# Kernel tuning notes

Hardware: AMD Instinct MI355X
Metric: run time of the kernel (lower is better)

## Reference

```python
import jax, jax.numpy as jnp
import numpy as np

RES = 0.1
TABLE = 2 ** 20
MOD_T = 201
HEADS = 8
M = 500_000
D = 120
PRIMES_NP = np.array([73856093, 19349669, 83492791], dtype=np.int64)
BMIN = np.array([-2.6, -8.1, 0.0], dtype=np.float32)
BMAX = np.array([4.6, 4.7, 3.1], dtype=np.float32)
CORNERS = [(0, 0, 0), (1, 0, 0), (0, 1, 0), (0, 0, 1), (1, 1, 0), (1, 0, 1), (0, 1, 1), (1, 1, 1)]


def _build_hash_table():
    # Mirror torch.arange / meshgrid voxel grid construction.
    xs = np.arange(BMIN[0], BMAX[0], RES, dtype=np.float32)
    ys = np.arange(BMIN[1], BMAX[1], RES, dtype=np.float32)
    zs = np.arange(BMIN[2], BMAX[2], RES, dtype=np.float32)
    gx, gy, gz = np.meshgrid(xs, ys, zs, indexing='ij')
    vox = np.stack([gx, gy, gz], axis=-1).reshape(-1, 3)
    grid = np.floor(vox / RES).astype(np.int64)
    h = np.remainder((grid * PRIMES_NP).sum(-1), TABLE)
    buf = np.full(TABLE, -1, dtype=np.int64)
    uh, first_idx = np.unique(h, return_index=True)
    buf[uh] = first_idx
    return buf, vox.shape[0]


def setup_inputs() -> dict:
    key = jax.random.key(0)
    ks = jax.random.split(key, 12)
    buf_np, total_voxels = _build_hash_table()
    u = jax.random.uniform(ks[0], (M, 3), dtype=jnp.float32)
    query_pts = jnp.asarray(BMIN) + u * jnp.asarray(BMAX - BMIN)
    query_times = jax.random.randint(ks[1], (M,), 0, 1000, dtype=jnp.int64)
    dynamic_features = jax.random.normal(ks[2], (total_voxels, D), dtype=jnp.float32) * 0.01
    time_embeddings = jax.random.normal(ks[3], (MOD_T, D), dtype=jnp.float32) * 0.01
    s = 1.0 / np.sqrt(D)
    Wq = jax.random.normal(ks[4], (D, D), dtype=jnp.float32) * s
    Wk = jax.random.normal(ks[5], (D, D), dtype=jnp.float32) * s
    Wv = jax.random.normal(ks[6], (D, D), dtype=jnp.float32) * s
    Wo = jax.random.normal(ks[7], (D, D), dtype=jnp.float32) * s
    bq = jnp.zeros((D,), jnp.float32)
    bk = jnp.zeros((D,), jnp.float32)
    bv = jnp.zeros((D,), jnp.float32)
    bo = jnp.zeros((D,), jnp.float32)
    return {
        'query_pts': query_pts, 'query_times': query_times,
        'dynamic_features': dynamic_features, 'time_embeddings': time_embeddings,
        'buffer_voxel_index': jnp.asarray(buf_np),
        'Wq': Wq, 'bq': bq, 'Wk': Wk, 'bk': bk, 'Wv': Wv, 'bv': bv, 'Wo': Wo, 'bo': bo,
    }


def _attn_fuse(feat, time_emb, Wq, bq, Wk, bk, Wv, bv, Wo, bo):
    # 2-token self-attention fusion: tokens = [voxel feature, time embedding]
    m, d = feat.shape
    dh = d // HEADS
    x = jnp.stack([feat, time_emb], axis=1)  # (M, 2, D)
    q = (x @ Wq + bq).reshape(m, 2, HEADS, dh)
    k = (x @ Wk + bk).reshape(m, 2, HEADS, dh)
    v = (x @ Wv + bv).reshape(m, 2, HEADS, dh)
    scores = jnp.einsum('mqhd,mkhd->mhqk', q, k) / jnp.sqrt(jnp.float32(dh))
    a = jax.nn.softmax(scores, axis=-1)
    o = jnp.einsum('mhqk,mkhd->mqhd', a, v).reshape(m, 2, d)
    o = o @ Wo + bo
    return o.mean(axis=1)  # (M, D)


def reference(query_pts, query_times, dynamic_features, time_embeddings,
              buffer_voxel_index, Wq, bq, Wk, bk, Wv, bv, Wo, bo):
    primes = jnp.asarray(PRIMES_NP)
    m = query_pts.shape[0]
    d = dynamic_features.shape[1]
    t_mod = jnp.remainder(query_times, MOD_T)

    gf = query_pts / RES
    gfl = jnp.floor(gf)
    frac = gf - gfl                      # (M, 3)
    base = gfl.astype(jnp.int64)         # (M, 3)

    accum = jnp.zeros((m, d), dtype=query_pts.dtype)
    for ox, oy, oz in CORNERS:           # fixed structural 8-corner loop
        cc = base + jnp.asarray([ox, oy, oz], dtype=jnp.int64)
        h = jnp.remainder((cc * primes).sum(-1), TABLE)
        vidx = buffer_voxel_index[h]
        valid = vidx >= 0
        wx = frac[:, 0] if ox else 1.0 - frac[:, 0]
        wy = frac[:, 1] if oy else 1.0 - frac[:, 1]
        wz = frac[:, 2] if oz else 1.0 - frac[:, 2]
        w = wx * wy * wz                 # (M,)
        f = dynamic_features[jnp.where(valid, vidx, 0)]
        accum = accum + jnp.where(valid[:, None], f * w[:, None], 0.0)

    time_emb = time_embeddings[t_mod]
    return _attn_fuse(accum, time_emb, Wq, bq, Wk, bk, Wv, bv, Wo, bo)
```

## Files before the change

kernel.cpp:

```cpp
#include <hip/hip_runtime.h>
#include <math.h>

#define M_D   120
#define MOD_T 201
#define TABLE_MASK 0xFFFFFu
#define INV_S 0.25819888974716115f

#define WS_TV  1608
#define WS_TQK 27336
#define WS_DYN16_BYTE (1ull << 20)

typedef float    f32x4 __attribute__((ext_vector_type(4)));
typedef uint32_t u32x4 __attribute__((ext_vector_type(4)));
typedef __fp16   f16x2v __attribute__((ext_vector_type(2)));
typedef __fp16   f16x8 __attribute__((ext_vector_type(8)));

union PK2 { f16x2v h; uint32_t u; };
union BFrag { f16x8 v; f16x2v h2[4]; uint32_t u[4]; };

__global__ void precomp_time(const float* __restrict__ temb,
                             const float* __restrict__ Wq, const float* __restrict__ bq,
                             const float* __restrict__ Wk, const float* __restrict__ bk,
                             const float* __restrict__ Wv, const float* __restrict__ bv,
                             float* __restrict__ ws) {
  const int t = blockIdx.x, np = threadIdx.x;
  const int h = np >> 4, m = np & 15;
  const bool valid = (m < 15);
  const int col = h * 15 + m;
  __shared__ float lq[128], lk[128];
  float q = 0.f, k = 0.f, v = 0.f;
  if (valid) {
    q = bq[col]; k = bk[col]; v = bv[col];
    const float* te = temb + t * M_D;
    for (int i = 0; i < M_D; ++i) {
      float x = te[i];
      q = fmaf(x, Wq[i * M_D + col], q);
      k = fmaf(x, Wk[i * M_D + col], k);
      v = fmaf(x, Wv[i * M_D + col], v);
    }
  }
  lq[np] = q; lk[np] = k;
  ws[WS_TV + t * 128 + np] = v;
  PK2 pk; pk.h[0] = (__fp16)(q * INV_S); pk.h[1] = (__fp16)k;
  ((uint32_t*)ws)[WS_TQK + t * 128 + np] = pk.u;
  __syncthreads();
  if (np < 8) {
    float s = 0.f;
    #pragma unroll
    for (int mm = 0; mm < 15; ++mm) s += lq[np * 16 + mm] * lk[np * 16 + mm];
    ws[t * 8 + np] = s * INV_S;
  }
}

__global__ void cvt_dyn(const float* __restrict__ dyn, __fp16* __restrict__ d16, int rows) {
  const int i = blockIdx.x * 256 + threadIdx.x;
  const int row = i >> 4, sub = i & 15;
  if (row < rows) {
    BFrag o;
    if (sub == 15) { o.u[0] = 0; o.u[1] = 0; o.u[2] = 0; o.u[3] = 0; }
    else {
      const float* src = dyn + (long)row * M_D + sub * 8;
      const f32x4 a = __builtin_nontemporal_load((const f32x4*)src);
      const f32x4 b = __builtin_nontemporal_load((const f32x4*)(src + 4));
      o.h2[0] = __builtin_amdgcn_cvt_pkrtz(a[0], a[1]);
      o.h2[1] = __builtin_amdgcn_cvt_pkrtz(a[2], a[3]);
      o.h2[2] = __builtin_amdgcn_cvt_pkrtz(b[0], b[1]);
      o.h2[3] = __builtin_amdgcn_cvt_pkrtz(b[2], b[3]);
    }
    *(f16x8*)(d16 + (long)row * 128 + sub * 8) = o.v;
  }
}

__launch_bounds__(256, 2)
__global__ void gather_feat(const float* __restrict__ qpts, const __fp16* __restrict__ dyn16,
                            const int* __restrict__ hbuf, __fp16* __restrict__ feat, int M) {
  const int l = threadIdx.x & 63, wv = threadIdx.x >> 6;
  const int g = l >> 4, pl = l & 15;
  const int T = (M + 15) >> 4;
  for (int tile = blockIdx.x * 4 + wv; tile < T; tile += gridDim.x * 4) {
    const int pid = (tile << 4) + pl;
    const int p = (pid < M) ? pid : (M - 1);
    const float px = qpts[3 * p], py = qpts[3 * p + 1], pz = qpts[3 * p + 2];
    const float gx = px / 0.1f, gy = py / 0.1f, gz = pz / 0.1f;
    const float fx = floorf(gx), fy = floorf(gy), fz = floorf(gz);
    const float rx = gx - fx, ry = gy - fy, rz = gz - fz;
    const int bx = (int)fx, by = (int)fy, bz = (int)fz;

    int voff[8]; float wcv[8];
    #pragma unroll
    for (int c = 0; c < 8; ++c) {
      const int ox = c & 1, oy = (c >> 1) & 1, oz = c >> 2;
      const uint32_t hh = (uint32_t)(bx + ox) * 73856093u +
                          (uint32_t)(by + oy) * 19349669u +
                          (uint32_t)(bz + oz) * 83492791u;
      const int vc = hbuf[hh & TABLE_MASK];
      const float wc = (ox ? rx : 1.f - rx) * (oy ? ry : 1.f - ry) * (oz ? rz : 1.f - rz);
      wcv[c] = (vc >= 0) ? wc : 0.f;
      voff[c] = ((vc >= 0) ? vc : 0) * 128 + g * 8;
    }

    __fp16* frow = feat + (long)pid * 128 + g * 8;
    f16x8 va[8], vb[8];
    #pragma unroll
    for (int c = 0; c < 8; ++c) va[c] = *(const f16x8*)(dyn16 + voff[c]);
    #pragma unroll
    for (int c = 0; c < 8; ++c) vb[c] = *(const f16x8*)(dyn16 + voff[c] + 32);

    auto PROC = [&](int kk, f16x8* vk) {
      f32x4 accA = {0, 0, 0, 0}, accB = {0, 0, 0, 0};
      #pragma unroll
      for (int c = 0; c < 8; ++c) {
        const float wc = wcv[c];
        const f16x8 v8 = vk[c];
        accA[0] = fmaf((float)v8[0], wc, accA[0]);
        accA[1] = fmaf((float)v8[1], wc, accA[1]);
        accA[2] = fmaf((float)v8[2], wc, accA[2]);
        accA[3] = fmaf((float)v8[3], wc, accA[3]);
        accB[0] = fmaf((float)v8[4], wc, accB[0]);
        accB[1] = fmaf((float)v8[5], wc, accB[1]);
        accB[2] = fmaf((float)v8[6], wc, accB[2]);
        accB[3] = fmaf((float)v8[7], wc, accB[3]);
      }
      if (kk == 3 && g == 3) accA[0] = 1.0f;
      BFrag o;
      o.h2[0] = __builtin_amdgcn_cvt_pkrtz(accA[0], accA[1]);
      o.h2[1] = __builtin_amdgcn_cvt_pkrtz(accA[2], accA[3]);
      o.h2[2] = __builtin_amdgcn_cvt_pkrtz(accB[0], accB[1]);
      o.h2[3] = __builtin_amdgcn_cvt_pkrtz(accB[2], accB[3]);
      if (pid < M) *(f16x8*)(frow + kk * 32) = o.v;
    };

    PROC(0, va);
    #pragma unroll
    for (int c = 0; c < 8; ++c) va[c] = *(const f16x8*)(dyn16 + voff[c] + 64);
    PROC(1, vb);
    #pragma unroll
    for (int c = 0; c < 8; ++c) vb[c] = *(const f16x8*)(dyn16 + voff[c] + 96);
    PROC(2, va);
    PROC(3, vb);
  }
}

__launch_bounds__(512, 2)
__global__ void mfma_main(const int* __restrict__ qtimes, const __fp16* __restrict__ feat,
                          const float* __restrict__ Wq, const float* __restrict__ bq,
                          const float* __restrict__ Wk, const float* __restrict__ bk,
                          const float* __restrict__ Wv, const float* __restrict__ bv,
                          const float* __restrict__ Wo, const float* __restrict__ bo,
                          const float* __restrict__ ws, float* __restrict__ out, int M) {
  __shared__ __align__(16) uint32_t wlds[4 * 8192];

  const int tid = threadIdx.x;
  for (int idx = tid; idx < 32768; idx += 512) {
    const int mat = idx >> 13, r = idx & 8191;
    const int nt = r >> 10, kk = (r >> 8) & 3, l = (r >> 2) & 63, d = r & 3;
    const int mm = l & 15;
    const int i0 = kk * 32 + ((l >> 4) << 3) + 2 * d;
    float v0 = 0.f, v1 = 0.f;
    if (mat < 3) {
      const float* W = (mat == 0) ? Wq : (mat == 1) ? Wk : Wv;
      const float* b = (mat == 0) ? bq : (mat == 1) ? bk : bv;
      if (mm < 15) {
        const int col = nt * 15 + mm;
        const int ia = i0, ib = i0 + 1;
        v0 = (ia < 120) ? W[ia * M_D + col] : (ia == 120 ? b[col] : 0.f);
        v1 = (ib < 120) ? W[ib * M_D + col] : (ib == 120 ? b[col] : 0.f);
        if (mat == 0) { v0 *= INV_S; v1 *= INV_S; }
      }
    } else {
      const int n = nt * 16 + mm;
      if (n < M_D) {
        #pragma unroll
        for (int e = 0; e < 2; ++e) {
          const int ip = i0 + e;
          const int hi = ip >> 4, mi = ip & 15;
          float vv = 0.f;
          if (mi < 15) vv = Wo[(hi * 15 + mi) * M_D + n];
          else if (ip == 15) vv = bo[n];
          if (e == 0) v0 = vv; else v1 = vv;
        }
      }
    }
    PK2 pk; pk.h[0] = (__fp16)v0; pk.h[1] = (__fp16)v1;
    wlds[idx] = pk.u;
  }
  __syncthreads();

  const uint32_t* wq = wlds;
  const uint32_t* wk = wlds + 8192;
  const uint32_t* wvm = wlds + 2 * 8192;
  const uint32_t* wo = wlds + 3 * 8192;

  const int l = tid & 63, wv = tid >> 6;
  const int g = l >> 4, pl = l & 15, c0 = g << 2;
  const float* S11 = ws;
  const float* TVt = ws + WS_TV;
  const uint32_t* TQK = (const uint32_t*)ws + WS_TQK;

  const int T = (M + 15) >> 4;
  for (int tile = blockIdx.x * 8 + wv; tile < T; tile += gridDim.x * 8) {
    const int pid = (tile << 4) + pl;
    const bool valid = (pid < M);
    const int p = valid ? pid : (M - 1);
    const int tm = qtimes[p] % MOD_T;

    BFrag bf[4];
    const __fp16* frow = feat + (long)p * 128 + g * 8;
    #pragma unroll
    for (int kk = 0; kk < 4; ++kk) bf[kk].v = *(const f16x8*)(frow + kk * 32);

    f32x4 tvv[8]; u32x4 tqk[8]; float s11v[8];
    #pragma unroll
    for (int nt = 0; nt < 8; ++nt) {
      tvv[nt] = *(const f32x4*)(TVt + tm * 128 + nt * 16 + c0);
      tqk[nt] = *(const u32x4*)(TQK + tm * 128 + nt * 16 + c0);
      s11v[nt] = S11[tm * 8 + nt];
    }

    f32x4 aq[8], ak[8], av[8];
    #pragma unroll
    for (int nt = 0; nt < 8; ++nt) {
      f32x4 zq = {0,0,0,0}, zk = {0,0,0,0}, zv = {0,0,0,0};
      #pragma unroll
      for (int kk = 0; kk < 4; ++kk) {
        const int off = nt * 1024 + kk * 256 + l * 4;
        f16x8 a0 = *(const f16x8*)(wq + off);
        f16x8 a1 = *(const f16x8*)(wk + off);
        f16x8 a2 = *(const f16x8*)(wvm + off);
        zq = __builtin_amdgcn_mfma_f32_16x16x32_f16(a0, bf[kk].v, zq, 0, 0, 0);
        zk = __builtin_amdgcn_mfma_f32_16x16x32_f16(a1, bf[kk].v, zk, 0, 0, 0);
        zv = __builtin_amdgcn_mfma_f32_16x16x32_f16(a2, bf[kk].v, zv, 0, 0, 0);
      }
      aq[nt] = zq; ak[nt] = zk; av[nt] = zv;
    }

    float a_[8], b_[8];
    #pragma unroll
    for (int nt = 0; nt < 8; ++nt) {
      float s00 = 0.f, s01 = 0.f, s10 = 0.f;
      #pragma unroll
      for (int r = 0; r < 4; ++r) {
        const float qv = aq[nt][r], kv = ak[nt][r];
        PK2 tt; tt.u = tqk[nt][r];
        const float tqs = (float)tt.h[0], tk = (float)tt.h[1];
        s00 = fmaf(qv, kv, s00);
        s01 = fmaf(qv, tk, s01);
        s10 = fmaf(tqs, kv, s10);
      }
      s00 += __shfl_xor(s00, 16); s00 += __shfl_xor(s00, 32);
      s01 += __shfl_xor(s01, 16); s01 += __shfl_xor(s01, 32);
      s10 += __shfl_xor(s10, 16); s10 += __shfl_xor(s10, 32);
      const float s11 = s11v[nt];
      const float m0 = fmaxf(s00, s01), m1 = fmaxf(s10, s11);
      const float e00 = __expf(s00 - m0), e01 = __expf(s01 - m0);
      const float e10 = __expf(s10 - m1), e11 = __expf(s11 - m1);
      const float r0 = 1.f / (e00 + e01), r1 = 1.f / (e10 + e11);
      a_[nt] = 0.5f * (e00 * r0 + e10 * r1);
      b_[nt] = 0.5f * (e01 * r0 + e11 * r1);
    }

    uint32_t cdw[8][2];
    #pragma unroll
    for (int nt = 0; nt < 8; ++nt) {
      f32x4 cv;
      #pragma unroll
      for (int r = 0; r < 4; ++r) cv[r] = a_[nt] * av[nt][r] + b_[nt] * tvv[nt][r];
      if (nt == 0 && g == 3) cv[3] = 1.0f;
      PK2 p0, p1;
      p0.h = __builtin_amdgcn_cvt_pkrtz(cv[0], cv[1]);
      p1.h = __builtin_amdgcn_cvt_pkrtz(cv[2], cv[3]);
      cdw[nt][0] = p0.u; cdw[nt][1] = p1.u;
    }

    const int src0 = pl | ((g & 1) << 5);
    const int src1 = src0 + 16;
    const bool hsel = (g >= 2);
    BFrag bco[4];
    #pragma unroll
    for (int kk = 0; kk < 4; ++kk) {
      #pragma unroll
      for (int d = 0; d < 4; ++d) {
        const int s = (d >= 2) ? src1 : src0;
        const int vlo = __shfl((int)cdw[2 * kk][d & 1], s, 64);
        const int vhi = __shfl((int)cdw[2 * kk + 1][d & 1], s, 64);
        bco[kk].u[d] = hsel ? (uint32_t)vhi : (uint32_t)vlo;
      }
    }

    float* orow = out + (long)p * M_D;
    #pragma unroll
    for (int nt = 0; nt < 8; ++nt) {
      f32x4 zo = {0,0,0,0};
      #pragma unroll
      for (int kk = 0; kk < 4; ++kk) {
        f16x8 a3 = *(const f16x8*)(wo + nt * 1024 + kk * 256 + l * 4);
        zo = __builtin_amdgcn_mfma_f32_16x16x32_f16(a3, bco[kk].v, zo, 0, 0, 0);
      }
      if (valid && (nt < 7 || g < 2))
        __builtin_nontemporal_store(zo, (f32x4*)(orow + nt * 16 + c0));
    }
  }
}

template <int USE16>
__launch_bounds__(512, 2)
__global__ void merged_main(const float* __restrict__ qpts, const int* __restrict__ qtimes,
                            const float* __restrict__ dyn,  const __fp16* __restrict__ dyn16,
                            const int* __restrict__ hbuf,
                            const float* __restrict__ Wq, const float* __restrict__ bq,
                            const float* __restrict__ Wk, const float* __restrict__ bk,
                            const float* __restrict__ Wv, const float* __restrict__ bv,
                            const float* __restrict__ Wo, const float* __restrict__ bo,
                            const float* __restrict__ ws, float* __restrict__ out, int M) {
  __shared__ __align__(16) uint32_t wlds[4 * 8192];
  const int tid = threadIdx.x;
  for (int idx = tid; idx < 32768; idx += 512) {
    const int mat = idx >> 13, r = idx & 8191;
    const int nt = r >> 10, kk = (r >> 8) & 3, l = (r >> 2) & 63, d = r & 3;
    const int mm = l & 15;
    const int i0 = kk * 32 + ((l >> 4) << 3) + 2 * d;
    float v0 = 0.f, v1 = 0.f;
    if (mat < 3) {
      const float* W = (mat == 0) ? Wq : (mat == 1) ? Wk : Wv;
      const float* b = (mat == 0) ? bq : (mat == 1) ? bk : bv;
      if (mm < 15) {
        const int col = nt * 15 + mm;
        const int ia = i0, ib = i0 + 1;
        v0 = (ia < 120) ? W[ia * M_D + col] : (ia == 120 ? b[col] : 0.f);
        v1 = (ib < 120) ? W[ib * M_D + col] : (ib == 120 ? b[col] : 0.f);
        if (mat == 0) { v0 *= INV_S; v1 *= INV_S; }
      }
    } else {
      const int n = nt * 16 + mm;
      if (n < M_D) {
        #pragma unroll
        for (int e = 0; e < 2; ++e) {
          const int ip = i0 + e;
          const int hi = ip >> 4, mi = ip & 15;
          float vv = 0.f;
          if (mi < 15) vv = Wo[(hi * 15 + mi) * M_D + n];
          else if (ip == 15) vv = bo[n];
          if (e == 0) v0 = vv; else v1 = vv;
        }
      }
    }
    PK2 pk; pk.h[0] = (__fp16)v0; pk.h[1] = (__fp16)v1;
    wlds[idx] = pk.u;
  }
  __syncthreads();

  const uint32_t* wq = wlds;
  const uint32_t* wk = wlds + 8192;
  const uint32_t* wvm = wlds + 2 * 8192;
  const uint32_t* wo = wlds + 3 * 8192;
  const int l = tid & 63, wv = tid >> 6;
  const int g = l >> 4, pl = l & 15, c0 = g << 2;
  const float* S11 = ws;
  const float* TVt = ws + WS_TV;
  const uint32_t* TQK = (const uint32_t*)ws + WS_TQK;

  const int T = (M + 15) >> 4;
  for (int tile = blockIdx.x * 8 + wv; tile < T; tile += gridDim.x * 8) {
    const int pid = (tile << 4) + pl;
    const int p = (pid < M) ? pid : (M - 1);
    const float px = qpts[3 * p], py = qpts[3 * p + 1], pz = qpts[3 * p + 2];
    const int tm = qtimes[p] % MOD_T;
    const float gx = px / 0.1f, gy = py / 0.1f, gz = pz / 0.1f;
    const float fx = floorf(gx), fy = floorf(gy), fz = floorf(gz);
    const float rx = gx - fx, ry = gy - fy, rz = gz - fz;
    const int bx = (int)fx, by = (int)fy, bz = (int)fz;
    const int i0g = g * 8;
    int voff[8]; float wcv[8];
    #pragma unroll
    for (int c = 0; c < 8; ++c) {
      const int ox = c & 1, oy = (c >> 1) & 1, oz = c >> 2;
      const uint32_t hh = (uint32_t)(bx + ox) * 73856093u +
                          (uint32_t)(by + oy) * 19349669u +
                          (uint32_t)(bz + oz) * 83492791u;
      const int vc = hbuf[hh & TABLE_MASK];
      const float wc = (ox ? rx : 1.f - rx) * (oy ? ry : 1.f - ry) * (oz ? rz : 1.f - rz);
      wcv[c] = (vc >= 0) ? wc : 0.f;
      const int vr = (vc >= 0) ? vc : 0;
      voff[c] = (USE16 ? vr * 128 : vr * M_D) + i0g;
    }
    BFrag bf[4];
    #pragma unroll
    for (int kk = 0; kk < 4; ++kk) {
      f32x4 accA = {0, 0, 0, 0}, accB = {0, 0, 0, 0};
      if (kk < 3 || g < 3) {
        #pragma unroll
        for (int c = 0; c < 8; ++c) {
          const float wc = wcv[c];
          if (USE16) {
            const f16x8 v8 = *(const f16x8*)(dyn16 + voff[c] + kk * 32);
            accA[0] = fmaf((float)v8[0], wc, accA[0]);
            accA[1] = fmaf((float)v8[1], wc, accA[1]);
            accA[2] = fmaf((float)v8[2], wc, accA[2]);
            accA[3] = fmaf((float)v8[3], wc, accA[3]);
            accB[0] = fmaf((float)v8[4], wc, accB[0]);
            accB[1] = fmaf((float)v8[5], wc, accB[1]);
            accB[2] = fmaf((float)v8[6], wc, accB[2]);
            accB[3] = fmaf((float)v8[7], wc, accB[3]);
          } else {
            const float* fr = dyn + voff[c];
            f32x4 lo4 = *(const f32x4*)(fr + kk * 32);
            f32x4 hi4 = *(const f32x4*)(fr + kk * 32 + 4);
            accA += lo4 * wc;
            accB += hi4 * wc;
          }
        }
      }
      if (kk == 3 && g == 3) accA[0] = 1.0f;
      bf[kk].h2[0] = __builtin_amdgcn_cvt_pkrtz(accA[0], accA[1]);
      bf[kk].h2[1] = __builtin_amdgcn_cvt_pkrtz(accA[2], accA[3]);
      bf[kk].h2[2] = __builtin_amdgcn_cvt_pkrtz(accB[0], accB[1]);
      bf[kk].h2[3] = __builtin_amdgcn_cvt_pkrtz(accB[2], accB[3]);
    }
    f32x4 tvv[8]; u32x4 tqk[8]; float s11v[8];
    #pragma unroll
    for (int nt = 0; nt < 8; ++nt) {
      tvv[nt] = *(const f32x4*)(TVt + tm * 128 + nt * 16 + c0);
      tqk[nt] = *(const u32x4*)(TQK + tm * 128 + nt * 16 + c0);
      s11v[nt] = S11[tm * 8 + nt];
    }
    f32x4 aq[8], ak[8], av[8];
    #pragma unroll
    for (int nt = 0; nt < 8; ++nt) {
      f32x4 zq = {0,0,0,0}, zk = {0,0,0,0}, zv = {0,0,0,0};
      #pragma unroll
      for (int kk = 0; kk < 4; ++kk) {
        const int off = nt * 1024 + kk * 256 + l * 4;
        f16x8 a0 = *(const f16x8*)(wq + off);
        f16x8 a1 = *(const f16x8*)(wk + off);
        f16x8 a2 = *(const f16x8*)(wvm + off);
        zq = __builtin_amdgcn_mfma_f32_16x16x32_f16(a0, bf[kk].v, zq, 0, 0, 0);
        zk = __builtin_amdgcn_mfma_f32_16x16x32_f16(a1, bf[kk].v, zk, 0, 0, 0);
        zv = __builtin_amdgcn_mfma_f32_16x16x32_f16(a2, bf[kk].v, zv, 0, 0, 0);
      }
      aq[nt] = zq; ak[nt] = zk; av[nt] = zv;
    }
    float a_[8], b_[8];
    #pragma unroll
    for (int nt = 0; nt < 8; ++nt) {
      float s00 = 0.f, s01 = 0.f, s10 = 0.f;
      #pragma unroll
      for (int r = 0; r < 4; ++r) {
        const float qv = aq[nt][r], kv = ak[nt][r];
        PK2 tt; tt.u = tqk[nt][r];
        s00 = fmaf(qv, kv, s00);
        s01 = fmaf(qv, (float)tt.h[1], s01);
        s10 = fmaf((float)tt.h[0], kv, s10);
      }
      s00 += __shfl_xor(s00, 16); s00 += __shfl_xor(s00, 32);
      s01 += __shfl_xor(s01, 16); s01 += __shfl_xor(s01, 32);
      s10 += __shfl_xor(s10, 16); s10 += __shfl_xor(s10, 32);
      const float s11 = s11v[nt];
      const float m0 = fmaxf(s00, s01), m1 = fmaxf(s10, s11);
      const float e00 = __expf(s00 - m0), e01 = __expf(s01 - m0);
      const float e10 = __expf(s10 - m1), e11 = __expf(s11 - m1);
      const float r0 = 1.f / (e00 + e01), r1 = 1.f / (e10 + e11);
      a_[nt] = 0.5f * (e00 * r0 + e10 * r1);
      b_[nt] = 0.5f * (e01 * r0 + e11 * r1);
    }
    uint32_t cdw[8][2];
    #pragma unroll
    for (int nt = 0; nt < 8; ++nt) {
      f32x4 cv;
      #pragma unroll
      for (int r = 0; r < 4; ++r) cv[r] = a_[nt] * av[nt][r] + b_[nt] * tvv[nt][r];
      if (nt == 0 && g == 3) cv[3] = 1.0f;
      PK2 p0, p1;
      p0.h = __builtin_amdgcn_cvt_pkrtz(cv[0], cv[1]);
      p1.h = __builtin_amdgcn_cvt_pkrtz(cv[2], cv[3]);
      cdw[nt][0] = p0.u; cdw[nt][1] = p1.u;
    }
    const int src0 = pl | ((g & 1) << 5);
    const int src1 = src0 + 16;
    const bool hsel = (g >= 2);
    BFrag bco[4];
    #pragma unroll
    for (int kk = 0; kk < 4; ++kk) {
      #pragma unroll
      for (int d = 0; d < 4; ++d) {
        const int s = (d >= 2) ? src1 : src0;
        const int vlo = __shfl((int)cdw[2 * kk][d & 1], s, 64);
        const int vhi = __shfl((int)cdw[2 * kk + 1][d & 1], s, 64);
        bco[kk].u[d] = hsel ? (uint32_t)vhi : (uint32_t)vlo;
      }
    }
    float* orow = out + (long)pid * M_D;
    #pragma unroll
    for (int nt = 0; nt < 8; ++nt) {
      f32x4 zo = {0,0,0,0};
      #pragma unroll
      for (int kk = 0; kk < 4; ++kk) {
        f16x8 a3 = *(const f16x8*)(wo + nt * 1024 + kk * 256 + l * 4);
        zo = __builtin_amdgcn_mfma_f32_16x16x32_f16(a3, bco[kk].v, zo, 0, 0, 0);
      }
      if (pid < M && (nt < 7 || g < 2))
        *(f32x4*)(orow + nt * 16 + c0) = zo;
    }
  }
}

extern "C" void kernel_launch(void* const* d_in, const int* in_sizes, int n_in,
                              void* d_out, int out_size, void* d_ws, size_t ws_size,
                              hipStream_t stream) {
  const float* qpts   = (const float*)d_in[0];
  const int*   qtimes = (const int*)d_in[1];
  const float* dyn    = (const float*)d_in[2];
  const float* temb   = (const float*)d_in[3];
  const int*   hbuf   = (const int*)d_in[4];
  const float* Wq = (const float*)d_in[5];
  const float* bq = (const float*)d_in[6];
  const float* Wk = (const float*)d_in[7];
  const float* bk = (const float*)d_in[8];
  const float* Wv = (const float*)d_in[9];
  const float* bv = (const float*)d_in[10];
  const float* Wo = (const float*)d_in[11];
  const float* bo = (const float*)d_in[12];
  float* out = (float*)d_out;
  float* ws  = (float*)d_ws;
  const int M = in_sizes[1];
  const int ndyn = in_sizes[2];
  const int rows = ndyn / M_D;

  hipLaunchKernelGGL(precomp_time, dim3(MOD_T), dim3(128), 0, stream,
                     temb, Wq, bq, Wk, bk, Wv, bv, ws);

  const size_t dyn16_bytes = (size_t)rows * 256;
  const size_t need16 = WS_DYN16_BYTE + dyn16_bytes;
  const size_t feat_off = (need16 + 255) & ~255ull;
  const size_t T16 = (size_t)(((M + 15) / 16) * 16);
  const size_t needF = feat_off + T16 * 256;

  if (ws_size >= need16) {
    __fp16* d16 = (__fp16*)((char*)d_ws + WS_DYN16_BYTE);
    const int nchunk = rows * 16;
    hipLaunchKernelGGL(cvt_dyn, dim3((nchunk + 255) / 256), dim3(256), 0, stream,
                       dyn, d16, rows);
    if (ws_size >= needF) {
      __fp16* feat = (__fp16*)((char*)d_ws + feat_off);
      hipLaunchKernelGGL(gather_feat, dim3(2048), dim3(256), 0, stream,
                         qpts, d16, hbuf, feat, M);
      hipLaunchKernelGGL(mfma_main, dim3(256), dim3(512), 0, stream,
                         qtimes, feat, Wq, bq, Wk, bk, Wv, bv, Wo, bo, ws, out, M);
    } else {
      hipLaunchKernelGGL(merged_main<1>, dim3(256), dim3(512), 0, stream,
                         qpts, qtimes, dyn, d16, hbuf,
                         Wq, bq, Wk, bk, Wv, bv, Wo, bo, ws, out, M);
    }
  } else {
    hipLaunchKernelGGL(merged_main<0>, dim3(256), dim3(512), 0, stream,
                       qpts, qtimes, dyn, (const __fp16*)nullptr, hbuf,
                       Wq, bq, Wk, bk, Wv, bv, Wo, bo, ws, out, M);
  }
}
```

Before: 1.089 ms.

## Stage time tables in LDS, stream packed weight fragments from global

```diff
diff --git a/kernel.cpp b/kernel.cpp
--- a/kernel.cpp
+++ b/kernel.cpp
@@ -6,13 +6,16 @@
 #define TABLE_MASK 0xFFFFFu
 #define INV_S 0.25819888974716115f
 
-#define WS_TV  1608
-#define WS_TQK 27336
+#define WS_TV   1608
+#define WS_TQK  27336
+#define WS_QF   53248
+#define WS_TVH_BYTE 344064ull
 #define WS_DYN16_BYTE (1ull << 20)
 
 typedef float    f32x4 __attribute__((ext_vector_type(4)));
 typedef uint32_t u32x4 __attribute__((ext_vector_type(4)));
 typedef __fp16   f16x2v __attribute__((ext_vector_type(2)));
+typedef __fp16   f16x4v __attribute__((ext_vector_type(4)));
 typedef __fp16   f16x8 __attribute__((ext_vector_type(8)));
 
 union PK2 { f16x2v h; uint32_t u; };
@@ -41,6 +44,7 @@
   }
   lq[np] = q; lk[np] = k;
   ws[WS_TV + t * 128 + np] = v;
+  ((__fp16*)((char*)ws + WS_TVH_BYTE))[t * 128 + np] = (__fp16)v;
   PK2 pk; pk.h[0] = (__fp16)(q * INV_S); pk.h[1] = (__fp16)k;
   ((uint32_t*)ws)[WS_TQK + t * 128 + np] = pk.u;
   __syncthreads();
@@ -50,6 +54,45 @@
     for (int mm = 0; mm < 15; ++mm) s += lq[np * 16 + mm] * lk[np * 16 + mm];
     ws[t * 8 + np] = s * INV_S;
   }
+}
+
+__global__ void pack_frags(const float* __restrict__ Wq, const float* __restrict__ bq,
+                           const float* __restrict__ Wk, const float* __restrict__ bk,
+                           const float* __restrict__ Wv, const float* __restrict__ bv,
+                           const float* __restrict__ Wo, const float* __restrict__ bo,
+                           float* __restrict__ ws) {
+  const int idx = blockIdx.x * 1024 + threadIdx.x;
+  const int mat = idx >> 13, r = idx & 8191;
+  const int nt = r >> 10, kk = (r >> 8) & 3, l = (r >> 2) & 63, d = r & 3;
+  const int mm = l & 15;
+  const int i0 = kk * 32 + ((l >> 4) << 3) + 2 * d;
+  float v0 = 0.f, v1 = 0.f;
+  if (mat < 3) {
+    const float* W = (mat == 0) ? Wq : (mat == 1) ? Wk : Wv;
+    const float* b = (mat == 0) ? bq : (mat == 1) ? bk : bv;
+    if (mm < 15) {
+      const int col = nt * 15 + mm;
+      const int ia = i0, ib = i0 + 1;
+      v0 = (ia < 120) ? W[ia * M_D + col] : (ia == 120 ? b[col] : 0.f);
+      v1 = (ib < 120) ? W[ib * M_D + col] : (ib == 120 ? b[col] : 0.f);
+      if (mat == 0) { v0 *= INV_S; v1 *= INV_S; }
+    }
+  } else {
+    const int n = nt * 16 + mm;
+    if (n < M_D) {
+      #pragma unroll
+      for (int e = 0; e < 2; ++e) {
+        const int ip = i0 + e;
+        const int hi = ip >> 4, mi = ip & 15;
+        float vv = 0.f;
+        if (mi < 15) vv = Wo[(hi * 15 + mi) * M_D + n];
+        else if (ip == 15) vv = bo[n];
+        if (e == 0) v0 = vv; else v1 = vv;
+      }
+    }
+  }
+  PK2 pk; pk.h[0] = (__fp16)v0; pk.h[1] = (__fp16)v1;
+  ((uint32_t*)ws)[WS_QF + idx] = pk.u;
 }
 
 __global__ void cvt_dyn(const float* __restrict__ dyn, __fp16* __restrict__ d16, int rows) {
@@ -143,59 +186,30 @@
 
 __launch_bounds__(512, 2)
 __global__ void mfma_main(const int* __restrict__ qtimes, const __fp16* __restrict__ feat,
-                          const float* __restrict__ Wq, const float* __restrict__ bq,
-                          const float* __restrict__ Wk, const float* __restrict__ bk,
-                          const float* __restrict__ Wv, const float* __restrict__ bv,
-                          const float* __restrict__ Wo, const float* __restrict__ bo,
                           const float* __restrict__ ws, float* __restrict__ out, int M) {
-  __shared__ __align__(16) uint32_t wlds[4 * 8192];
+  __shared__ __align__(16) char tlds_raw[160800];
+  uint32_t* tqk_lds = (uint32_t*)tlds_raw;
+  __fp16*   tvh_lds = (__fp16*)(tlds_raw + 102912);
+  float*    s11_lds = (float*)(tlds_raw + 154368);
 
   const int tid = threadIdx.x;
-  for (int idx = tid; idx < 32768; idx += 512) {
-    const int mat = idx >> 13, r = idx & 8191;
-    const int nt = r >> 10, kk = (r >> 8) & 3, l = (r >> 2) & 63, d = r & 3;
-    const int mm = l & 15;
-    const int i0 = kk * 32 + ((l >> 4) << 3) + 2 * d;
-    float v0 = 0.f, v1 = 0.f;
-    if (mat < 3) {
-      const float* W = (mat == 0) ? Wq : (mat == 1) ? Wk : Wv;
-      const float* b = (mat == 0) ? bq : (mat == 1) ? bk : bv;
-      if (mm < 15) {
-        const int col = nt * 15 + mm;
-        const int ia = i0, ib = i0 + 1;
-        v0 = (ia < 120) ? W[ia * M_D + col] : (ia == 120 ? b[col] : 0.f);
-        v1 = (ib < 120) ? W[ib * M_D + col] : (ib == 120 ? b[col] : 0.f);
-        if (mat == 0) { v0 *= INV_S; v1 *= INV_S; }
-      }
-    } else {
-      const int n = nt * 16 + mm;
-      if (n < M_D) {
-        #pragma unroll
-        for (int e = 0; e < 2; ++e) {
-          const int ip = i0 + e;
-          const int hi = ip >> 4, mi = ip & 15;
-          float vv = 0.f;
-          if (mi < 15) vv = Wo[(hi * 15 + mi) * M_D + n];
-          else if (ip == 15) vv = bo[n];
-          if (e == 0) v0 = vv; else v1 = vv;
-        }
-      }
-    }
-    PK2 pk; pk.h[0] = (__fp16)v0; pk.h[1] = (__fp16)v1;
-    wlds[idx] = pk.u;
+  {
+    const uint32_t* src_tqk = (const uint32_t*)ws + WS_TQK;
+    const uint32_t* src_tvh = (const uint32_t*)((const char*)ws + WS_TVH_BYTE);
+    uint32_t* dst_tvh = (uint32_t*)tvh_lds;
+    for (int i = tid; i < 25728; i += 512) tqk_lds[i] = src_tqk[i];
+    for (int i = tid; i < 12864; i += 512) dst_tvh[i] = src_tvh[i];
+    for (int i = tid; i < 1608; i += 512) s11_lds[i] = ws[i];
   }
   __syncthreads();
 
-  const uint32_t* wq = wlds;
-  const uint32_t* wk = wlds + 8192;
-  const uint32_t* wvm = wlds + 2 * 8192;
-  const uint32_t* wo = wlds + 3 * 8192;
+  const uint32_t* wqg = (const uint32_t*)ws + WS_QF;
+  const uint32_t* wkg = wqg + 8192;
+  const uint32_t* wvg = wqg + 16384;
+  const uint32_t* wog = wqg + 24576;
 
   const int l = tid & 63, wv = tid >> 6;
   const int g = l >> 4, pl = l & 15, c0 = g << 2;
-  const float* S11 = ws;
-  const float* TVt = ws + WS_TV;
-  const uint32_t* TQK = (const uint32_t*)ws + WS_TQK;
 
   const int T = (M + 15) >> 4;
   for (int tile = blockIdx.x * 8 + wv; tile < T; tile += gridDim.x * 8) {
@@ -212,9 +226,11 @@
     f32x4 tvv[8]; u32x4 tqk[8]; float s11v[8];
     #pragma unroll
     for (int nt = 0; nt < 8; ++nt) {
-      tvv[nt] = *(const f32x4*)(TVt + tm * 128 + nt * 16 + c0);
-      tqk[nt] = *(const u32x4*)(TQK + tm * 128 + nt * 16 + c0);
-      s11v[nt] = S11[tm * 8 + nt];
+      const f16x4v th = *(const f16x4v*)(tvh_lds + tm * 128 + nt * 16 + c0);
+      tvv[nt][0] = (float)th[0]; tvv[nt][1] = (float)th[1];
+      tvv[nt][2] = (float)th[2]; tvv[nt][3] = (float)th[3];
+      tqk[nt] = *(const u32x4*)(tqk_lds + tm * 128 + nt * 16 + c0);
+      s11v[nt] = s11_lds[tm * 8 + nt];
     }
 
     f32x4 aq[8], ak[8], av[8];
@@ -224,9 +240,9 @@
       #pragma unroll
       for (int kk = 0; kk < 4; ++kk) {
         const int off = nt * 1024 + kk * 256 + l * 4;
-        f16x8 a0 = *(const f16x8*)(wq + off);
-        f16x8 a1 = *(const f16x8*)(wk + off);
-        f16x8 a2 = *(const f16x8*)(wvm + off);
+        f16x8 a0 = *(const f16x8*)(wqg + off);
+        f16x8 a1 = *(const f16x8*)(wkg + off);
+        f16x8 a2 = *(const f16x8*)(wvg + off);
         zq = __builtin_amdgcn_mfma_f32_16x16x32_f16(a0, bf[kk].v, zq, 0, 0, 0);
         zk = __builtin_amdgcn_mfma_f32_16x16x32_f16(a1, bf[kk].v, zk, 0, 0, 0);
         zv = __builtin_amdgcn_mfma_f32_16x16x32_f16(a2, bf[kk].v, zv, 0, 0, 0);
@@ -293,11 +309,11 @@
       f32x4 zo = {0,0,0,0};
       #pragma unroll
       for (int kk = 0; kk < 4; ++kk) {
-        f16x8 a3 = *(const f16x8*)(wo + nt * 1024 + kk * 256 + l * 4);
+        f16x8 a3 = *(const f16x8*)(wog + nt * 1024 + kk * 256 + l * 4);
         zo = __builtin_amdgcn_mfma_f32_16x16x32_f16(a3, bco[kk].v, zo, 0, 0, 0);
       }
       if (valid && (nt < 7 || g < 2))
-        __builtin_nontemporal_store(zo, (f32x4*)(orow + nt * 16 + c0));
+        *(f32x4*)(orow + nt * 16 + c0) = zo;
     }
   }
 }
@@ -541,10 +557,12 @@
                        dyn, d16, rows);
     if (ws_size >= needF) {
       __fp16* feat = (__fp16*)((char*)d_ws + feat_off);
+      hipLaunchKernelGGL(pack_frags, dim3(32), dim3(1024), 0, stream,
+                         Wq, bq, Wk, bk, Wv, bv, Wo, bo, ws);
       hipLaunchKernelGGL(gather_feat, dim3(2048), dim3(256), 0, stream,
                          qpts, d16, hbuf, feat, M);
       hipLaunchKernelGGL(mfma_main, dim3(256), dim3(512), 0, stream,
-                         qtimes, feat, Wq, bq, Wk, bk, Wv, bv, Wo, bo, ws, out, M);
+                         qtimes, feat, ws, out, M);
     } else {
       hipLaunchKernelGGL(merged_main<1>, dim3(256), dim3(512), 0, stream,
                          qpts, qtimes, dyn, d16, hbuf,
```

Result: faster. 1.030 ms (-5.5%).
